# Performance work log

Hardware: AMD Instinct MI355X
Metric: run time of the kernel (lower is better)

## Reference

```python
import jax, jax.numpy as jnp
import numpy as np

B, T, D, H, E = 4, 2048, 1024, 4096, 8


def setup_inputs() -> dict:
    key = jax.random.key(0)
    ks = jax.random.split(key, 7)
    x = jax.random.normal(ks[0], (B, T, D), dtype=jnp.float32)
    # Gate: Linear(D, E)
    Wg = jax.random.normal(ks[1], (D, E), dtype=jnp.float32) / np.sqrt(D)
    bg = jax.random.normal(ks[2], (E,), dtype=jnp.float32) * 0.01
    # Experts: E x [Linear(D,H), ReLU, Linear(H,D)] (dropout inactive at eval)
    W1 = jax.random.normal(ks[3], (E, D, H), dtype=jnp.float32) / np.sqrt(D)
    b1 = jax.random.normal(ks[4], (E, H), dtype=jnp.float32) * 0.01
    W2 = jax.random.normal(ks[5], (E, H, D), dtype=jnp.float32) / np.sqrt(H)
    b2 = jax.random.normal(ks[6], (E, D), dtype=jnp.float32) * 0.01
    return {"x": x, "Wg": Wg, "bg": bg, "W1": W1, "b1": b1, "W2": W2, "b2": b2}


def reference(x, Wg, bg, W1, b1, W2, b2):
    # Gate + hard top-1 routing
    gate_scores = x @ Wg + bg                      # [B,T,E]
    top1 = jnp.argmax(gate_scores, axis=-1)        # [B,T]
    onehot = jax.nn.one_hot(top1, Wg.shape[-1], dtype=x.dtype)  # [B,T,E]
    # Dense: every expert MLP over all tokens (matches original's masked
    # formulation: x*mask == x on selected tokens, output re-masked).
    h = jax.nn.relu(jnp.einsum('btd,edh->beth', x, W1) + b1[None, :, None, :])
    y = jnp.einsum('beth,ehd->betd', h, W2) + b2[None, :, None, :]
    # Masked combine: keep only the token's chosen expert output
    out = jnp.einsum('betd,bte->btd', y, onehot)
    return out
```

## Files before the change

kernel.cpp:

```cpp
#include <hip/hip_runtime.h>
#include <hip/hip_bf16.h>
#include <stdint.h>

#define NTOK 8192
#define DDIM 1024
#define HDIM 4096
#define NEXP 8
#define MAXWL1 48
#define MAXWL2 72

typedef __attribute__((ext_vector_type(4))) float f32x4;
typedef __attribute__((ext_vector_type(8))) short s16x8;
typedef __attribute__((ext_vector_type(8))) unsigned short u16x8;

__device__ __forceinline__ unsigned short f2bf(float f) {
  union { float f; unsigned int u; } v; v.f = f;
  unsigned int u = v.u;
  u += 0x7FFFu + ((u >> 16) & 1u);
  return (unsigned short)(u >> 16);
}

typedef __attribute__((address_space(3))) unsigned char lds_u8;
typedef const __attribute__((address_space(1))) unsigned char glb_u8;

__device__ __forceinline__ void load_lds16(const void* g, void* l) {
  __builtin_amdgcn_global_load_lds((glb_u8*)g, (lds_u8*)l, 16, 0, 0);
}

__global__ __launch_bounds__(256) void gate_kernel(
    const float* __restrict__ x, const float* __restrict__ Wg,
    const float* __restrict__ bg, int* __restrict__ counts,
    int* __restrict__ lists) {
  const int lane = threadIdx.x & 63;
  const int tok = blockIdx.x * 4 + (threadIdx.x >> 6);
  const float* xr = x + (size_t)tok * DDIM;
  double acc[NEXP];
#pragma unroll
  for (int e = 0; e < NEXP; ++e) acc[e] = 0.0;
#pragma unroll 4
  for (int it = 0; it < DDIM / 64; ++it) {
    const int d = it * 64 + lane;
    const float xv = xr[d];
    const f32x4 w0 = *(const f32x4*)(Wg + (size_t)d * NEXP);
    const f32x4 w1 = *(const f32x4*)(Wg + (size_t)d * NEXP + 4);
#pragma unroll
    for (int j = 0; j < 4; ++j) {
      acc[j]     += (double)xv * (double)w0[j];
      acc[4 + j] += (double)xv * (double)w1[j];
    }
  }
#pragma unroll
  for (int e = 0; e < NEXP; ++e) {
    double v = acc[e];
#pragma unroll
    for (int off = 32; off > 0; off >>= 1) v += __shfl_xor(v, off, 64);
    acc[e] = v;
  }
  if (lane == 0) {
    int best = 0;
    double bv = acc[0] + (double)bg[0];
#pragma unroll
    for (int e = 1; e < NEXP; ++e) {
      const double v = acc[e] + (double)bg[e];
      if (v > bv) { bv = v; best = e; }
    }
    const int pos = atomicAdd(&counts[best], 1);
    lists[best * NTOK + pos] = tok;
  }
}

__global__ void offs_kernel(const int* __restrict__ counts, int* __restrict__ offs,
                            int* __restrict__ wl1, int* __restrict__ wl2) {
  int s = 0;
#pragma unroll
  for (int e = 0; e < NEXP; ++e) { offs[e] = s; s += counts[e]; }
  offs[NEXP] = s;
  int n1 = 0, n2 = 0;
  for (int e = 0; e < NEXP; ++e) {
    const int nb1 = (counts[e] + 255) >> 8;
    for (int b = 0; b < nb1; ++b) wl1[n1++] = (e << 20) | b;
    const int nb2 = (counts[e] + 127) >> 7;
    for (int b = 0; b < nb2; ++b) wl2[n2++] = (e << 20) | b;
  }
  offs[NEXP + 1] = n1;
  offs[NEXP + 2] = n2;
}

__global__ __launch_bounds__(256) void gather_conv_kernel(
    const float* __restrict__ x, const int* __restrict__ offs,
    const int* __restrict__ lists, int* __restrict__ stok,
    unsigned short* __restrict__ xbs) {
  const int p = blockIdx.x * 4 + (threadIdx.x >> 6);
  const int lane = threadIdx.x & 63;
  int e = 0;
#pragma unroll
  for (int k = 1; k < NEXP; ++k) e += (p >= offs[k]) ? 1 : 0;
  const int tok = lists[e * NTOK + (p - offs[e])];
  if (lane == 0) stok[p] = tok;
  const float* src = x + (size_t)tok * DDIM + lane * 16;
  unsigned short* dst = xbs + (size_t)p * DDIM + lane * 16;
#pragma unroll
  for (int q = 0; q < 2; ++q) {
    const f32x4 a = *(const f32x4*)(src + q * 8);
    const f32x4 b = *(const f32x4*)(src + q * 8 + 4);
    u16x8 o;
#pragma unroll
    for (int j = 0; j < 4; ++j) { o[j] = f2bf(a[j]); o[4 + j] = f2bf(b[j]); }
    *(u16x8*)(dst + q * 8) = o;
  }
}

__device__ __forceinline__ void transpose_tile(
    const float* __restrict__ ine, unsigned short* __restrict__ oute,
    int R, int C, int c0, int r0, int t) {
  __shared__ unsigned short T[64][66];
  const int tr = t >> 4, tc4 = (t & 15) * 4;
#pragma unroll
  for (int p = 0; p < 4; ++p) {
    const int r = tr + p * 16;
    const f32x4 v = *(const f32x4*)(ine + (size_t)(r0 + r) * C + c0 + tc4);
#pragma unroll
    for (int j = 0; j < 4; ++j) T[r][tc4 + j] = f2bf(v[j]);
  }
  __syncthreads();
  const int cc = t >> 3, rr8 = (t & 7) * 8;
#pragma unroll
  for (int p = 0; p < 2; ++p) {
    const int c = cc + p * 32;
    u16x8 o;
#pragma unroll
    for (int j = 0; j < 8; ++j) o[j] = T[rr8 + j][c];
    *(u16x8*)(oute + (size_t)(c0 + c) * R + r0 + rr8) = o;
  }
}

__global__ __launch_bounds__(256) void transpose_conv_kernel(
    const float* __restrict__ in, unsigned short* __restrict__ out,
    int R, int C) {
  const int e = blockIdx.z;
  transpose_tile(in + (size_t)e * R * C, out + (size_t)e * C * R, R, C,
                 blockIdx.x * 64, blockIdx.y * 64, threadIdx.x);
}

__global__ __launch_bounds__(256) void transpose_conv2_kernel(
    const float* __restrict__ W1, const float* __restrict__ W2,
    unsigned short* __restrict__ Wt1, unsigned short* __restrict__ Wt2) {
  const int id = blockIdx.x;
  if (id < 8192) {
    const int e = id >> 10, rem = id & 1023;
    const int cb = rem & 63, rb = rem >> 6;
    transpose_tile(W1 + (size_t)e * DDIM * HDIM, Wt1 + (size_t)e * HDIM * DDIM,
                   DDIM, HDIM, cb * 64, rb * 64, threadIdx.x);
  } else {
    const int id2 = id - 8192;
    const int e = id2 >> 10, rem = id2 & 1023;
    const int cb = rem & 15, rb = rem >> 4;
    transpose_tile(W2 + (size_t)e * HDIM * DDIM, Wt2 + (size_t)e * DDIM * HDIM,
                   HDIM, DDIM, cb * 64, rb * 64, threadIdx.x);
  }
}

template <int BM, int BN, int WM, int WN, int K, int N, int MAXWLT,
          bool COLFAST, bool FUSE1>
__global__ __launch_bounds__(512, 4) void ffn_kernel(
    const unsigned short* __restrict__ A, const unsigned short* __restrict__ Bt,
    const float* __restrict__ bias, const int* __restrict__ counts,
    const int* __restrict__ offs, const int* __restrict__ wl,
    const int* __restrict__ stok, unsigned short* __restrict__ outb,
    float* __restrict__ outf, int nwl_idx) {
  constexpr int MF = BM / (WM * 16);
  constexpr int NF = BN / (WN * 16);
  constexpr int ISS_A = BM / 128;
  constexpr int ISS_B = BN / 128;
  constexpr int NT = K / 32;
  constexpr int NCB = N / BN;
  constexpr int NWG = NCB * MAXWLT;
  static_assert((NWG & 7) == 0 && (NT & 1) == 0 && NT >= 4, "");
  static_assert(WM * WN == 8, "8 waves");

  const int d = blockIdx.x;
  const int logical = (d & 7) * (NWG / 8) + (d >> 3);
  int cb, wli;
  if constexpr (COLFAST) { cb = logical % NCB; wli = logical / NCB; }
  else                   { cb = logical / MAXWLT; wli = logical % MAXWLT; }
  if (wli >= offs[nwl_idx]) return;
  const int col0 = cb * BN;
  const int wle = wl[wli];
  const int e = wle >> 20;
  const int bx = wle & 0xFFFFF;
  const int cnt = counts[e];
  const int row0 = offs[e] + bx * BM;

  __shared__ __align__(16) unsigned short As0[BM * 32], Bs0[BN * 32];
  __shared__ __align__(16) unsigned short As1[BM * 32], Bs1[BN * 32];

  const int tid = threadIdx.x;
  const int lane = tid & 63;
  const int w = tid >> 6;
  const int wm = w / WN;
  const int wn = w % WN;
  const int fr = lane & 15;
  const int fj = lane >> 4;

  const int swsrc = ((tid & 3) ^ ((tid >> 3) & 3)) * 8;
  const int rb = tid >> 2;
  const unsigned short* srcA[ISS_A];
#pragma unroll
  for (int i = 0; i < ISS_A; ++i) {
    int gr = row0 + i * 128 + rb;
    if (gr > NTOK - 1) gr = NTOK - 1;
    srcA[i] = A + (size_t)gr * K + swsrc;
  }
  const unsigned short* Bte = Bt + (size_t)e * N * K;
  const unsigned short* srcB[ISS_B];
#pragma unroll
  for (int i = 0; i < ISS_B; ++i)
    srcB[i] = Bte + (size_t)(col0 + i * 128 + rb) * K + swsrc;

  const int js = (fj ^ ((fr >> 1) & 3)) * 8;

  f32x4 acc[MF][NF];
#pragma unroll
  for (int m = 0; m < MF; ++m)
#pragma unroll
    for (int n = 0; n < NF; ++n) acc[m][n] = f32x4{0.f, 0.f, 0.f, 0.f};

  auto stage = [&](unsigned short* dA, unsigned short* dB, int kel) {
#pragma unroll
    for (int i = 0; i < ISS_A; ++i)
      load_lds16(srcA[i] + kel, dA + i * 4096 + tid * 8);
#pragma unroll
    for (int i = 0; i < ISS_B; ++i)
      load_lds16(srcB[i] + kel, dB + i * 4096 + tid * 8);
  };

  auto phase = [&](const unsigned short* pA, const unsigned short* pB,
                   unsigned short* nA, unsigned short* nB, int knext,
                   bool do_stage) {
    asm volatile("s_waitcnt vmcnt(0)" ::: "memory");
    __builtin_amdgcn_s_barrier();
    asm volatile("" ::: "memory");
    s16x8 af[MF], bf[NF];
#pragma unroll
    for (int m = 0; m < MF; ++m)
      af[m] = *(const s16x8*)(pA + (wm * MF * 16 + m * 16 + fr) * 32 + js);
#pragma unroll
    for (int n = 0; n < NF; ++n)
      bf[n] = *(const s16x8*)(pB + (wn * NF * 16 + n * 16 + fr) * 32 + js);
    if (do_stage) stage(nA, nB, knext);
    __builtin_amdgcn_s_setprio(1);
#pragma unroll
    for (int m = 0; m < MF; ++m)
#pragma unroll
      for (int n = 0; n < NF; ++n)
        acc[m][n] = __builtin_amdgcn_mfma_f32_16x16x32_bf16(af[m], bf[n],
                                                            acc[m][n], 0, 0, 0);
    __builtin_amdgcn_s_setprio(0);
  };

  stage(As0, Bs0, 0);
#pragma unroll 1
  for (int t = 0; t < NT - 2; t += 2) {
    phase(As0, Bs0, As1, Bs1, (t + 1) * 32, true);
    phase(As1, Bs1, As0, Bs0, (t + 2) * 32, true);
  }
  phase(As0, Bs0, As1, Bs1, (NT - 1) * 32, true);
  phase(As1, Bs1, nullptr, nullptr, 0, false);

#pragma unroll
  for (int n = 0; n < NF; ++n) {
    const int col = col0 + wn * NF * 16 + n * 16 + fr;
    const float bv = bias[e * N + col];
#pragma unroll
    for (int m = 0; m < MF; ++m) {
#pragma unroll
      for (int j = 0; j < 4; ++j) {
        const int rl = wm * MF * 16 + m * 16 + fj * 4 + j;
        if (bx * BM + rl < cnt) {
          if constexpr (FUSE1) {
            outb[(size_t)(row0 + rl) * N + col] = f2bf(fmaxf(acc[m][n][j] + bv, 0.f));
          } else {
            outf[(size_t)stok[row0 + rl] * N + col] = acc[m][n][j] + bv;
          }
        }
      }
    }
  }
}

extern "C" void kernel_launch(void* const* d_in, const int* in_sizes, int n_in,
                              void* d_out, int out_size, void* d_ws, size_t ws_size,
                              hipStream_t stream) {
  (void)in_sizes; (void)n_in; (void)out_size;
  const float* x  = (const float*)d_in[0];
  const float* Wg = (const float*)d_in[1];
  const float* bg = (const float*)d_in[2];
  const float* W1 = (const float*)d_in[3];
  const float* b1 = (const float*)d_in[4];
  const float* W2 = (const float*)d_in[5];
  const float* b2 = (const float*)d_in[6];
  float* out = (float*)d_out;

  char* ws = (char*)d_ws;
  const size_t OFF_CNT = 0;
  const size_t OFF_OFF = 128;
  const size_t OFF_WL1 = 256;
  const size_t OFF_WL2 = 256 + MAXWL1 * 4;
  const size_t OFF_LST = 1024;
  const size_t OFF_STK = OFF_LST + (size_t)NEXP * NTOK * 4;
  const size_t OFF_XBS = OFF_STK + (size_t)NTOK * 4;
  const size_t OFF_HS  = OFF_XBS + (size_t)NTOK * DDIM * 2;
  const size_t OFF_WT1 = OFF_HS + (size_t)NTOK * HDIM * 2;
  const size_t SZ_W    = (size_t)NEXP * DDIM * HDIM * 2;
  const size_t OFF_WT2 = OFF_WT1 + SZ_W;
  const size_t NEED_SMALL = OFF_WT1 + SZ_W;
  const size_t NEED_BIG   = OFF_WT2 + SZ_W;
  if (ws_size < NEED_SMALL) return;
  const bool big = (ws_size >= NEED_BIG);

  int* counts = (int*)(ws + OFF_CNT);
  int* offs   = (int*)(ws + OFF_OFF);
  int* wl1    = (int*)(ws + OFF_WL1);
  int* wl2    = (int*)(ws + OFF_WL2);
  int* lists  = (int*)(ws + OFF_LST);
  int* stok   = (int*)(ws + OFF_STK);
  unsigned short* xbs = (unsigned short*)(ws + OFF_XBS);
  unsigned short* Hs  = (unsigned short*)(ws + OFF_HS);
  unsigned short* Wt1 = (unsigned short*)(ws + OFF_WT1);
  unsigned short* Wt2 = big ? (unsigned short*)(ws + OFF_WT2) : Wt1;

  hipMemsetAsync(counts, 0, 128, stream);
  gate_kernel<<<NTOK / 4, 256, 0, stream>>>(x, Wg, bg, counts, lists);
  offs_kernel<<<1, 1, 0, stream>>>(counts, offs, wl1, wl2);
  gather_conv_kernel<<<NTOK / 4, 256, 0, stream>>>(x, offs, lists, stok, xbs);

  if (big) {
    transpose_conv2_kernel<<<16384, 256, 0, stream>>>(W1, W2, Wt1, Wt2);
    ffn_kernel<256, 128, 4, 2, DDIM, HDIM, MAXWL1, false, true>
        <<<dim3((HDIM / 128) * MAXWL1), 512, 0, stream>>>(
            xbs, Wt1, b1, counts, offs, wl1, stok, Hs, nullptr, NEXP + 1);
    ffn_kernel<128, 256, 2, 4, HDIM, DDIM, MAXWL2, true, false>
        <<<dim3((DDIM / 256) * MAXWL2), 512, 0, stream>>>(
            Hs, Wt2, b2, counts, offs, wl2, stok, nullptr, out, NEXP + 2);
  } else {
    transpose_conv_kernel<<<dim3(HDIM / 64, DDIM / 64, NEXP), 256, 0, stream>>>(
        W1, Wt1, DDIM, HDIM);
    ffn_kernel<256, 128, 4, 2, DDIM, HDIM, MAXWL1, false, true>
        <<<dim3((HDIM / 128) * MAXWL1), 512, 0, stream>>>(
            xbs, Wt1, b1, counts, offs, wl1, stok, Hs, nullptr, NEXP + 1);
    transpose_conv_kernel<<<dim3(DDIM / 64, HDIM / 64, NEXP), 256, 0, stream>>>(
        W2, Wt1, HDIM, DDIM);
    ffn_kernel<128, 256, 2, 4, HDIM, DDIM, MAXWL2, true, false>
        <<<dim3((DDIM / 256) * MAXWL2), 512, 0, stream>>>(
            Hs, Wt1, b2, counts, offs, wl2, stok, nullptr, out, NEXP + 2);
  }
}
```

Before: 466.3 us.

## Overlap weight transposes with gather and first FFN via merged kernels

```diff
diff --git a/kernel.cpp b/kernel.cpp
--- a/kernel.cpp
+++ b/kernel.cpp
@@ -8,6 +8,7 @@
 #define NEXP 8
 #define MAXWL1 48
 #define MAXWL2 72
+#define FFN1_GRID ((HDIM / 128) * MAXWL1)
 
 typedef __attribute__((ext_vector_type(4))) float f32x4;
 typedef __attribute__((ext_vector_type(8))) short s16x8;
@@ -86,41 +87,16 @@
   offs[NEXP + 2] = n2;
 }
 
-__global__ __launch_bounds__(256) void gather_conv_kernel(
-    const float* __restrict__ x, const int* __restrict__ offs,
-    const int* __restrict__ lists, int* __restrict__ stok,
-    unsigned short* __restrict__ xbs) {
-  const int p = blockIdx.x * 4 + (threadIdx.x >> 6);
-  const int lane = threadIdx.x & 63;
-  int e = 0;
-#pragma unroll
-  for (int k = 1; k < NEXP; ++k) e += (p >= offs[k]) ? 1 : 0;
-  const int tok = lists[e * NTOK + (p - offs[e])];
-  if (lane == 0) stok[p] = tok;
-  const float* src = x + (size_t)tok * DDIM + lane * 16;
-  unsigned short* dst = xbs + (size_t)p * DDIM + lane * 16;
-#pragma unroll
-  for (int q = 0; q < 2; ++q) {
-    const f32x4 a = *(const f32x4*)(src + q * 8);
-    const f32x4 b = *(const f32x4*)(src + q * 8 + 4);
-    u16x8 o;
-#pragma unroll
-    for (int j = 0; j < 4; ++j) { o[j] = f2bf(a[j]); o[4 + j] = f2bf(b[j]); }
-    *(u16x8*)(dst + q * 8) = o;
-  }
-}
-
 __device__ __forceinline__ void transpose_tile(
     const float* __restrict__ ine, unsigned short* __restrict__ oute,
-    int R, int C, int c0, int r0, int t) {
-  __shared__ unsigned short T[64][66];
+    int R, int C, int c0, int r0, int t, unsigned short* Tb) {
   const int tr = t >> 4, tc4 = (t & 15) * 4;
 #pragma unroll
   for (int p = 0; p < 4; ++p) {
     const int r = tr + p * 16;
     const f32x4 v = *(const f32x4*)(ine + (size_t)(r0 + r) * C + c0 + tc4);
 #pragma unroll
-    for (int j = 0; j < 4; ++j) T[r][tc4 + j] = f2bf(v[j]);
+    for (int j = 0; j < 4; ++j) Tb[r * 66 + tc4 + j] = f2bf(v[j]);
   }
   __syncthreads();
   const int cc = t >> 3, rr8 = (t & 7) * 8;
@@ -129,7 +105,7 @@
     const int c = cc + p * 32;
     u16x8 o;
 #pragma unroll
-    for (int j = 0; j < 8; ++j) o[j] = T[rr8 + j][c];
+    for (int j = 0; j < 8; ++j) o[j] = Tb[(rr8 + j) * 66 + c];
     *(u16x8*)(oute + (size_t)(c0 + c) * R + r0 + rr8) = o;
   }
 }
@@ -137,37 +113,59 @@
 __global__ __launch_bounds__(256) void transpose_conv_kernel(
     const float* __restrict__ in, unsigned short* __restrict__ out,
     int R, int C) {
+  __shared__ __align__(16) unsigned short T[64 * 66];
   const int e = blockIdx.z;
   transpose_tile(in + (size_t)e * R * C, out + (size_t)e * C * R, R, C,
-                 blockIdx.x * 64, blockIdx.y * 64, threadIdx.x);
-}
-
-__global__ __launch_bounds__(256) void transpose_conv2_kernel(
-    const float* __restrict__ W1, const float* __restrict__ W2,
-    unsigned short* __restrict__ Wt1, unsigned short* __restrict__ Wt2) {
-  const int id = blockIdx.x;
-  if (id < 8192) {
+                 blockIdx.x * 64, blockIdx.y * 64, threadIdx.x, T);
+}
+
+__global__ __launch_bounds__(512) void gather_w1t_kernel(
+    const float* __restrict__ x, const int* __restrict__ offs,
+    const int* __restrict__ lists, int* __restrict__ stok,
+    unsigned short* __restrict__ xbs, const float* __restrict__ W1,
+    unsigned short* __restrict__ Wt1) {
+  __shared__ __align__(16) unsigned short TT[2][64 * 66];
+  const int bid = blockIdx.x;
+  const int tid = threadIdx.x;
+  if (bid < NTOK / 8) {
+    const int p = bid * 8 + (tid >> 6);
+    const int lane = tid & 63;
+    int e = 0;
+#pragma unroll
+    for (int k = 1; k < NEXP; ++k) e += (p >= offs[k]) ? 1 : 0;
+    const int tok = lists[e * NTOK + (p - offs[e])];
+    if (lane == 0) stok[p] = tok;
+    const float* src = x + (size_t)tok * DDIM + lane * 16;
+    unsigned short* dst = xbs + (size_t)p * DDIM + lane * 16;
+#pragma unroll
+    for (int q = 0; q < 2; ++q) {
+      const f32x4 a = *(const f32x4*)(src + q * 8);
+      const f32x4 b = *(const f32x4*)(src + q * 8 + 4);
+      u16x8 o;
+#pragma unroll
+      for (int j = 0; j < 4; ++j) { o[j] = f2bf(a[j]); o[4 + j] = f2bf(b[j]); }
+      *(u16x8*)(dst + q * 8) = o;
+    }
+  } else {
+    const int id = (bid - NTOK / 8) * 2 + (tid >> 8);
+    const int t = tid & 255;
     const int e = id >> 10, rem = id & 1023;
     const int cb = rem & 63, rb = rem >> 6;
     transpose_tile(W1 + (size_t)e * DDIM * HDIM, Wt1 + (size_t)e * HDIM * DDIM,
-                   DDIM, HDIM, cb * 64, rb * 64, threadIdx.x);
-  } else {
-    const int id2 = id - 8192;
-    const int e = id2 >> 10, rem = id2 & 1023;
-    const int cb = rem & 15, rb = rem >> 4;
-    transpose_tile(W2 + (size_t)e * HDIM * DDIM, Wt2 + (size_t)e * DDIM * HDIM,
-                   HDIM, DDIM, cb * 64, rb * 64, threadIdx.x);
+                   DDIM, HDIM, cb * 64, rb * 64, t, TT[tid >> 8]);
   }
 }
 
 template <int BM, int BN, int WM, int WN, int K, int N, int MAXWLT,
           bool COLFAST, bool FUSE1>
-__global__ __launch_bounds__(512, 4) void ffn_kernel(
-    const unsigned short* __restrict__ A, const unsigned short* __restrict__ Bt,
-    const float* __restrict__ bias, const int* __restrict__ counts,
-    const int* __restrict__ offs, const int* __restrict__ wl,
-    const int* __restrict__ stok, unsigned short* __restrict__ outb,
-    float* __restrict__ outf, int nwl_idx) {
+__device__ __forceinline__ void ffn_body(
+    int d, const unsigned short* __restrict__ A,
+    const unsigned short* __restrict__ Bt, const float* __restrict__ bias,
+    const int* __restrict__ counts, const int* __restrict__ offs,
+    const int* __restrict__ wl, const int* __restrict__ stok,
+    unsigned short* __restrict__ outb, float* __restrict__ outf, int nwl_idx,
+    unsigned short* As0, unsigned short* Bs0,
+    unsigned short* As1, unsigned short* Bs1) {
   constexpr int MF = BM / (WM * 16);
   constexpr int NF = BN / (WN * 16);
   constexpr int ISS_A = BM / 128;
@@ -178,7 +176,6 @@
   static_assert((NWG & 7) == 0 && (NT & 1) == 0 && NT >= 4, "");
   static_assert(WM * WN == 8, "8 waves");
 
-  const int d = blockIdx.x;
   const int logical = (d & 7) * (NWG / 8) + (d >> 3);
   int cb, wli;
   if constexpr (COLFAST) { cb = logical % NCB; wli = logical / NCB; }
@@ -191,9 +188,6 @@
   const int cnt = counts[e];
   const int row0 = offs[e] + bx * BM;
 
-  __shared__ __align__(16) unsigned short As0[BM * 32], Bs0[BN * 32];
-  __shared__ __align__(16) unsigned short As1[BM * 32], Bs1[BN * 32];
-
   const int tid = threadIdx.x;
   const int lane = tid & 63;
   const int w = tid >> 6;
@@ -286,6 +280,45 @@
       }
     }
   }
+}
+
+__global__ __launch_bounds__(512, 4) void ffn1_w2t_kernel(
+    const unsigned short* __restrict__ A, const unsigned short* __restrict__ Bt,
+    const float* __restrict__ bias, const int* __restrict__ counts,
+    const int* __restrict__ offs, const int* __restrict__ wl,
+    const int* __restrict__ stok, unsigned short* __restrict__ Hs,
+    const float* __restrict__ W2, unsigned short* __restrict__ Wt2) {
+  __shared__ __align__(16) unsigned short As0[256 * 32], Bs0[128 * 32];
+  __shared__ __align__(16) unsigned short As1[256 * 32], Bs1[128 * 32];
+  const int bid = blockIdx.x;
+  if (bid < FFN1_GRID) {
+    ffn_body<256, 128, 4, 2, DDIM, HDIM, MAXWL1, false, true>(
+        bid, A, Bt, bias, counts, offs, wl, stok, Hs, nullptr, NEXP + 1,
+        As0, Bs0, As1, Bs1);
+  } else {
+    const int id = (bid - FFN1_GRID) * 2 + (threadIdx.x >> 8);
+    const int t = threadIdx.x & 255;
+    const int e = id >> 10, rem = id & 1023;
+    const int cb = rem & 15, rb = rem >> 4;
+    transpose_tile(W2 + (size_t)e * HDIM * DDIM, Wt2 + (size_t)e * DDIM * HDIM,
+                   HDIM, DDIM, cb * 64, rb * 64, t,
+                   (threadIdx.x >= 256) ? As1 : As0);
+  }
+}
+
+template <int BM, int BN, int WM, int WN, int K, int N, int MAXWLT,
+          bool COLFAST, bool FUSE1>
+__global__ __launch_bounds__(512, 4) void ffn_kernel(
+    const unsigned short* __restrict__ A, const unsigned short* __restrict__ Bt,
+    const float* __restrict__ bias, const int* __restrict__ counts,
+    const int* __restrict__ offs, const int* __restrict__ wl,
+    const int* __restrict__ stok, unsigned short* __restrict__ outb,
+    float* __restrict__ outf, int nwl_idx) {
+  __shared__ __align__(16) unsigned short As0[BM * 32], Bs0[BN * 32];
+  __shared__ __align__(16) unsigned short As1[BM * 32], Bs1[BN * 32];
+  ffn_body<BM, BN, WM, WN, K, N, MAXWLT, COLFAST, FUSE1>(
+      blockIdx.x, A, Bt, bias, counts, offs, wl, stok, outb, outf, nwl_idx,
+      As0, Bs0, As1, Bs1);
 }
 
 extern "C" void kernel_launch(void* const* d_in, const int* in_sizes, int n_in,
@@ -332,26 +365,21 @@
   hipMemsetAsync(counts, 0, 128, stream);
   gate_kernel<<<NTOK / 4, 256, 0, stream>>>(x, Wg, bg, counts, lists);
   offs_kernel<<<1, 1, 0, stream>>>(counts, offs, wl1, wl2);
-  gather_conv_kernel<<<NTOK / 4, 256, 0, stream>>>(x, offs, lists, stok, xbs);
+
+  gather_w1t_kernel<<<NTOK / 8 + 4096, 512, 0, stream>>>(
+      x, offs, lists, stok, xbs, W1, Wt1);
 
   if (big) {
-    transpose_conv2_kernel<<<16384, 256, 0, stream>>>(W1, W2, Wt1, Wt2);
+    ffn1_w2t_kernel<<<FFN1_GRID + 4096, 512, 0, stream>>>(
+        xbs, Wt1, b1, counts, offs, wl1, stok, Hs, W2, Wt2);
+  } else {
     ffn_kernel<256, 128, 4, 2, DDIM, HDIM, MAXWL1, false, true>
-        <<<dim3((HDIM / 128) * MAXWL1), 512, 0, stream>>>(
-            xbs, Wt1, b1, counts, offs, wl1, stok, Hs, nullptr, NEXP + 1);
-    ffn_kernel<128, 256, 2, 4, HDIM, DDIM, MAXWL2, true, false>
-        <<<dim3((DDIM / 256) * MAXWL2), 512, 0, stream>>>(
-            Hs, Wt2, b2, counts, offs, wl2, stok, nullptr, out, NEXP + 2);
-  } else {
-    transpose_conv_kernel<<<dim3(HDIM / 64, DDIM / 64, NEXP), 256, 0, stream>>>(
-        W1, Wt1, DDIM, HDIM);
-    ffn_kernel<256, 128, 4, 2, DDIM, HDIM, MAXWL1, false, true>
-        <<<dim3((HDIM / 128) * MAXWL1), 512, 0, stream>>>(
+        <<<dim3(FFN1_GRID), 512, 0, stream>>>(
             xbs, Wt1, b1, counts, offs, wl1, stok, Hs, nullptr, NEXP + 1);
     transpose_conv_kernel<<<dim3(DDIM / 64, HDIM / 64, NEXP), 256, 0, stream>>>(
         W2, Wt1, HDIM, DDIM);
-    ffn_kernel<128, 256, 2, 4, HDIM, DDIM, MAXWL2, true, false>
-        <<<dim3((DDIM / 256) * MAXWL2), 512, 0, stream>>>(
-            Hs, Wt1, b2, counts, offs, wl2, stok, nullptr, out, NEXP + 2);
-  }
-}
+  }
+  ffn_kernel<128, 256, 2, 4, HDIM, DDIM, MAXWL2, true, false>
+      <<<dim3((DDIM / 256) * MAXWL2), 512, 0, stream>>>(
+          Hs, Wt2, b2, counts, offs, wl2, stok, nullptr, out, NEXP + 2);
+}
```

Result: faster. 434.0 us (-6.9%).
